# Kernel tuning notes

Hardware: AMD Instinct MI355X
Metric: run time of the kernel (lower is better)

The kernel has to match this reference:

```python
import jax, jax.numpy as jnp
import numpy as np

K_TOP = 128
NORM_TYPE = 'l2'  # 'l2' | 'l1' | 'avg'

def _norm(x, norm_type):
    if norm_type == 'l2':
        return jnp.sum(jnp.square(x), axis=2)
    if norm_type == 'l1':
        return jnp.sum(jnp.abs(x), axis=2)
    return jnp.sum(x, axis=2)  # 'avg'

def setup_inputs() -> dict:
    key = jax.random.key(0)
    x = jax.random.normal(key, (64, 8192, 256), dtype=jnp.float32)
    return {"x": x}

def reference(x) -> jnp.ndarray:
    # x: [B, N, D]
    norms = _norm(x, NORM_TYPE)                      # [B, N]
    _, idx = jax.lax.top_k(norms, K_TOP)             # [B, k], descending-norm order
    # gather the k selected embedding rows per batch element -> [B, k, D]
    return jnp.take_along_axis(x, idx[:, :, None], axis=1)
```

## Files before the change

### kernel.cpp

```cpp
#include <hip/hip_runtime.h>

constexpr int B = 64;
constexpr int N = 8192;
constexpr int D = 256;
constexpr int K = 128;

__global__ __launch_bounds__(256) void norms_kernel(const float* __restrict__ x,
                                                    float* __restrict__ norms) {
    const int row  = blockIdx.x * 4 + (threadIdx.x >> 6);
    const int lane = threadIdx.x & 63;
    const float4 v = reinterpret_cast<const float4*>(x + (size_t)row * D)[lane];
    float s = v.x * v.x + v.y * v.y + v.z * v.z + v.w * v.w;
    #pragma unroll
    for (int off = 32; off > 0; off >>= 1)
        s += __shfl_xor(s, off, 64);
    if (lane == 0) norms[row] = s;
}

__global__ __launch_bounds__(1024) void topk_gather_kernel(const float* __restrict__ norms,
                                                           const float* __restrict__ x,
                                                           float* __restrict__ out) {
    __shared__ unsigned long long keys[N];
    __shared__ unsigned int hist[256];
    __shared__ unsigned int seg[32];
    __shared__ unsigned long long s_prefix;
    __shared__ unsigned int s_krem;
    __shared__ int s_done;
    __shared__ unsigned int s_cnt;
    __shared__ unsigned long long cand[K];
    __shared__ int sorted_src[K];

    const int b    = blockIdx.x;
    const int tid  = threadIdx.x;
    const int lane = tid & 63;
    const float* nb = norms + (size_t)b * N;

    for (int i = tid; i < N; i += 1024) {
        const unsigned int bits = __float_as_uint(nb[i]);
        keys[i] = ((unsigned long long)bits << 32) | (unsigned int)(N - 1 - i);
    }
    if (tid == 0) { s_prefix = 0ull; s_krem = K; s_done = 0; s_cnt = 0u; }
    __syncthreads();

    for (int p = 7; p >= 0; --p) {
        if (s_done) break;
        const int shift = p * 8;
        const unsigned long long prefix = s_prefix;
        const unsigned int       krem   = s_krem;
        if (tid < 256) hist[tid] = 0u;
        __syncthreads();

        if (p == 7) {
            for (int i = tid; i < N; i += 1024) {
                const unsigned int d = (unsigned int)(keys[i] >> 56);
                unsigned long long rem = __ballot(true);
                while (rem) {
                    const int leader = __ffsll(rem) - 1;
                    const unsigned int dl = __shfl(d, leader, 64);
                    const unsigned long long grp = __ballot(d == dl);
                    if (lane == leader) atomicAdd(&hist[dl], (unsigned int)__popcll(grp));
                    rem &= ~grp;
                }
            }
        } else {
            for (int i = tid; i < N; i += 1024) {
                const unsigned long long key = keys[i];
                if ((key >> (shift + 8)) == (prefix >> (shift + 8)))
                    atomicAdd(&hist[(unsigned int)(key >> shift) & 255u], 1u);
            }
        }
        __syncthreads();

        if (tid < 32) {
            unsigned int s = 0;
            #pragma unroll
            for (int d2 = 0; d2 < 8; ++d2) s += hist[tid * 8 + d2];
            seg[tid] = s;
        }
        __syncthreads();

        if (tid < 256) {
            unsigned int cnt_gt = 0;
            const int hiSeg = (tid >> 3) + 1;
            for (int s2 = hiSeg; s2 < 32; ++s2) cnt_gt += seg[s2];
            for (int d2 = tid + 1; d2 < hiSeg * 8; ++d2) cnt_gt += hist[d2];
            const unsigned int h = hist[tid];
            if (cnt_gt < krem && krem <= cnt_gt + h) {
                s_prefix = prefix | ((unsigned long long)tid << shift);
                s_krem   = krem - cnt_gt;
                if (h == krem - cnt_gt) s_done = 1;
            }
        }
        __syncthreads();
    }

    const unsigned long long T = s_prefix;
    for (int i = tid; i < N; i += 1024) {
        const unsigned long long key = keys[i];
        if (key >= T) {
            const unsigned int pos = atomicAdd(&s_cnt, 1u);
            cand[pos] = key;
        }
    }
    __syncthreads();

    if (tid < K) {
        const unsigned long long key = cand[tid];
        int rank = 0;
        for (int j = 0; j < K; ++j) rank += (cand[j] > key) ? 1 : 0;
        sorted_src[rank] = N - 1 - (int)(key & 0xFFFFFFFFu);
    }
    __syncthreads();

    for (int r = tid >> 6; r < K; r += 16) {
        const int src = sorted_src[r];
        const float4 v = reinterpret_cast<const float4*>(x + ((size_t)b * N + src) * D)[lane];
        reinterpret_cast<float4*>(out + ((size_t)b * K + r) * D)[lane] = v;
    }
}

extern "C" void kernel_launch(void* const* d_in, const int* in_sizes, int n_in,
                              void* d_out, int out_size, void* d_ws, size_t ws_size,
                              hipStream_t stream) {
    const float* x = (const float*)d_in[0];
    float* out = (float*)d_out;
    float* norms = (float*)d_ws;

    norms_kernel<<<B * N / 4, 256, 0, stream>>>(x, norms);
    topk_gather_kernel<<<B, 1024, 0, stream>>>(norms, x, out);
}
```

Baseline: 125.7 us.

## Fuse norm computation with per-chunk top-K preselection to shrink final select

The norm kernel now processes 256-row chunks per block. Each block stores key/index pairs in shared memory and ranks them by brute force, emitting that chunk's top 128 candidates. The final per-batch radix select then works on 4096 candidates instead of 8192 norms, which cuts the serial work in the 64-block second kernel. The cost is that each wave now loads 64 rows one after another, which may lower memory-level parallelism in the bandwidth-bound first pass, and each block adds an O(256²) shared-memory ranking step.

```diff
diff --git a/kernel.cpp b/kernel.cpp
--- a/kernel.cpp
+++ b/kernel.cpp
@@ -4,41 +4,63 @@
 constexpr int N = 8192;
 constexpr int D = 256;
 constexpr int K = 128;
+constexpr int CHUNKS = 32;
+constexpr int RPC = N / CHUNKS;
+constexpr int NCAND = CHUNKS * K;
 
-__global__ __launch_bounds__(256) void norms_kernel(const float* __restrict__ x,
-                                                    float* __restrict__ norms) {
-    const int row  = blockIdx.x * 4 + (threadIdx.x >> 6);
-    const int lane = threadIdx.x & 63;
-    const float4 v = reinterpret_cast<const float4*>(x + (size_t)row * D)[lane];
-    float s = v.x * v.x + v.y * v.y + v.z * v.z + v.w * v.w;
-    #pragma unroll
-    for (int off = 32; off > 0; off >>= 1)
-        s += __shfl_xor(s, off, 64);
-    if (lane == 0) norms[row] = s;
+__global__ __launch_bounds__(256) void norm_select_kernel(const float* __restrict__ x,
+                                                          unsigned long long* __restrict__ cand) {
+    __shared__ unsigned long long skeys[RPC];
+    const int bid   = blockIdx.x;
+    const int batch = bid >> 5;
+    const int chunk = bid & (CHUNKS - 1);
+    const int w     = threadIdx.x >> 6;
+    const int lane  = threadIdx.x & 63;
+    const size_t rowbase = (size_t)batch * N + (size_t)chunk * RPC;
+
+    const int lrow0 = w * 64;
+    for (int it = 0; it < 64; ++it) {
+        const int lrow = lrow0 + it;
+        const float4 v = reinterpret_cast<const float4*>(x + (rowbase + lrow) * D)[lane];
+        float s = v.x * v.x + v.y * v.y + v.z * v.z + v.w * v.w;
+        #pragma unroll
+        for (int off = 32; off > 0; off >>= 1)
+            s += __shfl_xor(s, off, 64);
+        if (lane == 0) {
+            const int grow = chunk * RPC + lrow;
+            skeys[lrow] = ((unsigned long long)__float_as_uint(s) << 32)
+                        | (unsigned int)(N - 1 - grow);
+        }
+    }
+    __syncthreads();
+
+    const unsigned long long mine = skeys[threadIdx.x];
+    int rank = 0;
+    for (int j = 0; j < RPC; ++j)
+        rank += (skeys[j] > mine) ? 1 : 0;
+    if (rank < K)
+        cand[(size_t)bid * K + rank] = mine;
 }
 
-__global__ __launch_bounds__(1024) void topk_gather_kernel(const float* __restrict__ norms,
+__global__ __launch_bounds__(1024) void topk_gather_kernel(const unsigned long long* __restrict__ cand_in,
                                                            const float* __restrict__ x,
                                                            float* __restrict__ out) {
-    __shared__ unsigned long long keys[N];
+    __shared__ unsigned long long keys[NCAND];
     __shared__ unsigned int hist[256];
     __shared__ unsigned int seg[32];
     __shared__ unsigned long long s_prefix;
     __shared__ unsigned int s_krem;
     __shared__ int s_done;
     __shared__ unsigned int s_cnt;
-    __shared__ unsigned long long cand[K];
+    __shared__ unsigned long long sel[K];
     __shared__ int sorted_src[K];
 
     const int b    = blockIdx.x;
     const int tid  = threadIdx.x;
     const int lane = tid & 63;
-    const float* nb = norms + (size_t)b * N;
 
-    for (int i = tid; i < N; i += 1024) {
-        const unsigned int bits = __float_as_uint(nb[i]);
-        keys[i] = ((unsigned long long)bits << 32) | (unsigned int)(N - 1 - i);
-    }
+    for (int i = tid; i < NCAND; i += 1024)
+        keys[i] = cand_in[(size_t)b * NCAND + i];
     if (tid == 0) { s_prefix = 0ull; s_krem = K; s_done = 0; s_cnt = 0u; }
     __syncthreads();
 
@@ -51,7 +73,7 @@
         __syncthreads();
 
         if (p == 7) {
-            for (int i = tid; i < N; i += 1024) {
+            for (int i = tid; i < NCAND; i += 1024) {
                 const unsigned int d = (unsigned int)(keys[i] >> 56);
                 unsigned long long rem = __ballot(true);
                 while (rem) {
@@ -63,7 +85,7 @@
                 }
             }
         } else {
-            for (int i = tid; i < N; i += 1024) {
+            for (int i = tid; i < NCAND; i += 1024) {
                 const unsigned long long key = keys[i];
                 if ((key >> (shift + 8)) == (prefix >> (shift + 8)))
                     atomicAdd(&hist[(unsigned int)(key >> shift) & 255u], 1u);
@@ -95,19 +117,19 @@
     }
 
     const unsigned long long T = s_prefix;
-    for (int i = tid; i < N; i += 1024) {
+    for (int i = tid; i < NCAND; i += 1024) {
         const unsigned long long key = keys[i];
         if (key >= T) {
             const unsigned int pos = atomicAdd(&s_cnt, 1u);
-            cand[pos] = key;
+            sel[pos] = key;
         }
     }
     __syncthreads();
 
     if (tid < K) {
-        const unsigned long long key = cand[tid];
+        const unsigned long long key = sel[tid];
         int rank = 0;
-        for (int j = 0; j < K; ++j) rank += (cand[j] > key) ? 1 : 0;
+        for (int j = 0; j < K; ++j) rank += (sel[j] > key) ? 1 : 0;
         sorted_src[rank] = N - 1 - (int)(key & 0xFFFFFFFFu);
     }
     __syncthreads();
@@ -124,8 +146,8 @@
                               hipStream_t stream) {
     const float* x = (const float*)d_in[0];
     float* out = (float*)d_out;
-    float* norms = (float*)d_ws;
+    unsigned long long* cand = (unsigned long long*)d_ws;
 
-    norms_kernel<<<B * N / 4, 256, 0, stream>>>(x, norms);
-    topk_gather_kernel<<<B, 1024, 0, stream>>>(norms, x, out);
+    norm_select_kernel<<<B * CHUNKS, 256, 0, stream>>>(x, cand);
+    topk_gather_kernel<<<B, 1024, 0, stream>>>(cand, x, out);
 }
```

After: 123.9 us. About the same (-1.4%).
